# Kernel tuning notes

Hardware: AMD Instinct MI355X
Metric: run time of the kernel (lower is better)

The kernel has to match this reference:

```python
import jax, jax.numpy as jnp
import numpy as np

RADIUS = 0.2  # ball_query_radius
K = 64        # max_group_size


def _xavier(key, out_c, in_c):
    lim = float(np.sqrt(6.0 / (in_c + out_c)))
    return jax.random.uniform(key, (out_c, in_c), jnp.float32, -lim, lim)


def setup_inputs() -> dict:
    key = jax.random.key(0)
    ks = jax.random.split(key, 9)
    B, N, C_in, C_out = 8, 4096, 64, 256
    h = C_out // 2
    return {
        "points": jax.random.uniform(ks[0], (B, 3, N), jnp.float32),
        "point_features": jax.random.normal(ks[1], (B, C_in, N), jnp.float32),
        # point_point_net: Conv2d(3,C_in,1) -> ReLU -> Conv2d(C_in,C_in,1) -> ReLU -> Conv2d(C_in,h,1)
        "pw1": _xavier(ks[2], C_in, 3), "pb1": jnp.zeros(C_in, jnp.float32),
        "pw2": _xavier(ks[3], C_in, C_in), "pb2": jnp.zeros(C_in, jnp.float32),
        "pw3": _xavier(ks[4], h, C_in), "pb3": jnp.zeros(h, jnp.float32),
        # feature_point_net: Conv2d(C_in,C_in,1) -> ReLU -> Conv2d(C_in,C_in,1) -> ReLU -> Conv2d(C_in,h,1)
        "fw1": _xavier(ks[5], C_in, C_in), "fb1": jnp.zeros(C_in, jnp.float32),
        "fw2": _xavier(ks[6], C_in, C_in), "fb2": jnp.zeros(C_in, jnp.float32),
        "fw3": _xavier(ks[7], h, C_in), "fb3": jnp.zeros(h, jnp.float32),
    }


def _fps(pts, M):
    """Farthest point sampling: pts [N,3] -> M int32 indices (first pick = 0)."""
    N = pts.shape[0]

    def step(carry, _):
        mind, last = carry
        d = jnp.sum((pts - pts[last]) ** 2, axis=-1)
        mind = jnp.minimum(mind, d)
        nxt = jnp.argmax(mind).astype(jnp.int32)
        return (mind, nxt), last

    init = (jnp.full((N,), jnp.inf, pts.dtype), jnp.int32(0))
    _, idx = jax.lax.scan(step, init, None, length=M)
    return idx


def _ball_group(cent, pts):
    """cent [M,3], pts [N,3] -> first K in-radius neighbor indices [M,K] (padded with first hit)."""
    N = pts.shape[0]
    d2 = jnp.sum((cent[:, None, :] - pts[None, :, :]) ** 2, axis=-1)  # [M,N]
    score = jnp.where(d2 <= RADIUS * RADIUS, jnp.arange(N, dtype=jnp.int32), N)
    neg_top, _ = jax.lax.top_k(-score, K)     # K smallest scores = first K in-radius point ids
    sel = -neg_top                            # [M,K]
    sel = jnp.where(sel < N, sel, sel[:, :1]) # pad misses with first valid (centroid itself, dist 0)
    return sel


def _mlp3(x, w1, b1, w2, b2, w3, b3):
    """1x1 Conv2d stack applied along the channel axis; x [B,M,K,C]."""
    h = jax.nn.relu(jnp.einsum('bmkc,oc->bmko', x, w1) + b1)
    h = jax.nn.relu(jnp.einsum('bmkc,oc->bmko', h, w2) + b2)
    return jnp.einsum('bmkc,oc->bmko', h, w3) + b3


def reference(points, point_features, pw1, pb1, pw2, pb2, pw3, pb3,
              fw1, fb1, fw2, fb2, fw3, fb3):
    B, _, N = points.shape
    M = N // 4
    pts = points.transpose(0, 2, 1)            # [B,N,3]
    feats = point_features.transpose(0, 2, 1)  # [B,N,C]

    idx = jax.vmap(lambda p: _fps(p, M))(pts)                 # [B,M]
    cent = jnp.take_along_axis(pts, idx[:, :, None], axis=1)  # [B,M,3]
    sel = jax.vmap(_ball_group)(cent, pts)                    # [B,M,K]

    gpts = jax.vmap(lambda p, s: p[s])(pts, sel)              # [B,M,K,3]
    rel = gpts - cent[:, :, None, :]                          # local coords around centroid
    gfeat = jax.vmap(lambda f, s: f[s])(feats, sel)           # [B,M,K,C]

    p_out = jnp.max(_mlp3(rel, pw1, pb1, pw2, pb2, pw3, pb3), axis=2)    # [B,M,h]
    f_out = jnp.max(_mlp3(gfeat, fw1, fb1, fw2, fb2, fw3, fb3), axis=2)  # [B,M,h]

    centroid_features = jnp.concatenate([f_out, p_out], axis=-1).transpose(0, 2, 1)  # [B,C_out,M]
    centroids = cent.reshape(B, 3, M)  # replicates torch .view(B,3,-1) on the flat [B*M,3] buffer
    return centroids, centroid_features
```

## Files before the change

kernel.cpp:

```cpp
#include <hip/hip_runtime.h>
#include <hip/hip_bf16.h>

#define BB   8
#define NN   4096
#define MM   1024
#define KK   64
#define CIN  64
#define HH   128

#define R2F 0.039999999105930328f

#define NPROD (BB + (BB * NN) / 256)
#define H2SU  36
#define SMEMF 21504

static __device__ __forceinline__ float rnd_bf16(float v) {
    return __bfloat162float(__float2bfloat16(v));
}
static __device__ __forceinline__ unsigned int bf16bits(float v) {
    unsigned int u = __float_as_uint(v);
    return (u + 0x7FFFu + ((u >> 16) & 1u)) >> 16;
}
static __device__ __forceinline__ void wavefence() {
    __builtin_amdgcn_wave_barrier();
    __threadfence_block();
    __builtin_amdgcn_wave_barrier();
}

__global__ __launch_bounds__(256) void fused_kernel(
    const float* __restrict__ pts,
    float* __restrict__ centf,
    float* __restrict__ outc,
    const float* __restrict__ feat,
    const float* __restrict__ fw1, const float* __restrict__ fb1,
    const float* __restrict__ fw2, const float* __restrict__ fb2,
    const float* __restrict__ fw3, const float* __restrict__ fb3,
    __hip_bfloat16* __restrict__ fout,
    const float* __restrict__ pw1, const float* __restrict__ pb1,
    const float* __restrict__ pw2, const float* __restrict__ pb2,
    const float* __restrict__ pw3, const float* __restrict__ pb3,
    float* __restrict__ outf,
    unsigned int* __restrict__ flags)
{
    __shared__ float smem[SMEMF];
    __shared__ unsigned long long akey[4];
    const int t = threadIdx.x;

    if (blockIdx.x < BB) {
        const int b = blockIdx.x;
        float* lx = smem;
        float* ly = smem + NN;
        float* lz = smem + 2 * NN;

        const float* px = pts + (size_t)b * 3 * NN;
        float x[16], y[16], z[16], mind[16];
#pragma unroll
        for (int i = 0; i < 16; ++i) {
            int p = t + i * 256;
            x[i] = px[p];
            y[i] = px[NN + p];
            z[i] = px[2 * NN + p];
            lx[p] = x[i]; ly[p] = y[i]; lz[p] = z[i];
            mind[i] = 3.4e38f;
        }
        if (t < 4) akey[t] = 0ULL;
        __syncthreads();

        float bx = lx[0], by = ly[0], bz = lz[0];

        for (int j = 0; j < MM; ++j) {
            if (t == 0) {
                int o = (b * MM + j) * 3;
                centf[o]    = bx; centf[o + 1] = by; centf[o + 2] = bz;
                outc[o]     = rnd_bf16(bx);
                outc[o + 1] = rnd_bf16(by);
                outc[o + 2] = rnd_bf16(bz);
                if ((j & 15) == 15)
                    __hip_atomic_store(&flags[b], (unsigned int)(j + 1),
                                       __ATOMIC_RELEASE, __HIP_MEMORY_SCOPE_AGENT);
                akey[(j + 2) & 3] = 0ULL;
            }
            float bd = -1.0f; int bi = 0;
#pragma unroll
            for (int i = 0; i < 16; ++i) {
                float dx = x[i] - bx, dy = y[i] - by, dz = z[i] - bz;
                float d = __fadd_rn(__fadd_rn(__fmul_rn(dx, dx), __fmul_rn(dy, dy)),
                                    __fmul_rn(dz, dz));
                float md = fminf(mind[i], d);
                mind[i] = md;
                if (md > bd) { bd = md; bi = t + i * 256; }
            }
            unsigned long long key =
                ((unsigned long long)__float_as_uint(bd) << 32) |
                (unsigned long long)(0xFFFFFFFFu - (unsigned)bi);
            atomicMax(&akey[j & 3], key);
            __syncthreads();
            unsigned long long bk = akey[j & 3];
            int best = (int)(0xFFFFFFFFu - (unsigned)(bk & 0xFFFFFFFFULL));
            bx = lx[best]; by = ly[best]; bz = lz[best];
        }
    } else if (blockIdx.x < NPROD) {
        float* w1 = smem;
        float* w2 = smem + CIN * CIN;
        for (int i = t; i < CIN * CIN; i += 256) { w1[i] = fw1[i]; w2[i] = fw2[i]; }
        __syncthreads();

        const int gid = (blockIdx.x - BB) * 256 + t;
        const int b = gid >> 12, n = gid & (NN - 1);
        const float* fp = feat + (size_t)b * CIN * NN + n;

        float f[CIN];
#pragma unroll
        for (int c = 0; c < CIN; ++c) f[c] = fp[(size_t)c * NN];

        float h1[CIN];
        for (int o = 0; o < CIN; ++o) {
            float acc = fb1[o];
#pragma unroll
            for (int c = 0; c < CIN; ++c) acc = fmaf(f[c], w1[o * CIN + c], acc);
            h1[o] = fmaxf(acc, 0.f);
        }
        float h2[CIN];
        for (int o = 0; o < CIN; ++o) {
            float acc = fb2[o];
#pragma unroll
            for (int c = 0; c < CIN; ++c) acc = fmaf(h1[c], w2[o * CIN + c], acc);
            h2[o] = fmaxf(acc, 0.f);
        }
        __hip_bfloat16* op = fout + (size_t)gid * HH;
        for (int o = 0; o < HH; ++o) {
            float acc = fb3[o];
#pragma unroll
            for (int c = 0; c < CIN; ++c) acc = fmaf(h2[c], fw3[o * CIN + c], acc);
            op[o] = __float2bfloat16(acc);
        }
        __threadfence();
        __syncthreads();
        if (t == 0)
            __hip_atomic_fetch_add(&flags[8], 1u,
                                   __ATOMIC_RELEASE, __HIP_MEMORY_SCOPE_AGENT);
    } else {
        const int wv = t >> 6, lane = t & 63;
        unsigned int* h2w = ((unsigned int*)smem) + wv * (KK * H2SU);
        int* selw = ((int*)smem) + 4 * (KK * H2SU) + wv * KK;

        const int idx = blockIdx.x - NPROD;
        const int b = idx & 7;
        const int m = (idx >> 3) * 4 + wv;
        const int g = b * MM + m;

        while (__hip_atomic_load(&flags[b], __ATOMIC_RELAXED,
                                 __HIP_MEMORY_SCOPE_AGENT) <= (unsigned)m)
            __builtin_amdgcn_s_sleep(8);
        (void)__hip_atomic_load(&flags[b], __ATOMIC_ACQUIRE,
                                __HIP_MEMORY_SCOPE_AGENT);

        const float* pts_b = pts + (size_t)b * 3 * NN;
        const float cx = centf[(size_t)g * 3];
        const float cy = centf[(size_t)g * 3 + 1];
        const float cz = centf[(size_t)g * 3 + 2];

        int cnt = 0, first = 0;
        bool have_first = false;
        float fx[4], fy[4], fz[4];
#pragma unroll
        for (int q = 0; q < 4; ++q) {
            int p = q * 64 + lane;
            fx[q] = pts_b[p]; fy[q] = pts_b[NN + p]; fz[q] = pts_b[2 * NN + p];
        }
        for (int base = 0; base < NN; base += 256) {
#pragma unroll
            for (int q = 0; q < 4; ++q) {
                const int cb = base + q * 64;
                float vx = fx[q], vy = fy[q], vz = fz[q];
                const int pre = cb + 256 + lane;
                if (pre < NN) {
                    fx[q] = pts_b[pre]; fy[q] = pts_b[NN + pre]; fz[q] = pts_b[2 * NN + pre];
                }
                float dx = vx - cx, dy = vy - cy, dz = vz - cz;
                float d2 = __fadd_rn(__fadd_rn(__fmul_rn(dx, dx), __fmul_rn(dy, dy)),
                                     __fmul_rn(dz, dz));
                bool in = (d2 <= R2F);
                unsigned long long mask = __ballot(in);
                if (!have_first && mask != 0ULL) {
                    first = cb + (int)__builtin_ctzll(mask);
                    have_first = true;
                }
                int pos = cnt + (int)__popcll(mask & ((1ULL << lane) - 1ULL));
                if (in && pos < KK) selw[pos] = cb + lane;
                cnt += (int)__popcll(mask);
            }
        }
        if (cnt < KK) {
            for (int q = cnt + lane; q < KK; q += 64) selw[q] = first;
        }
        wavefence();

        const int s = selw[lane];
        float* ob = outf + (size_t)b * 256 * MM + m;

        {
            const float x = pts_b[s]          - cx;
            const float y = pts_b[NN + s]     - cy;
            const float z = pts_b[2 * NN + s] - cz;
            float h1[CIN];
#pragma unroll
            for (int o = 0; o < CIN; ++o) {
                float acc = pb1[o];
                acc = fmaf(x, pw1[o * 3 + 0], acc);
                acc = fmaf(y, pw1[o * 3 + 1], acc);
                acc = fmaf(z, pw1[o * 3 + 2], acc);
                h1[o] = fmaxf(acc, 0.f);
            }
            for (int o8 = 0; o8 < CIN / 8; ++o8) {
                float a[8];
#pragma unroll
                for (int q = 0; q < 8; ++q) a[q] = pb2[o8 * 8 + q];
                for (int c = 0; c < CIN; ++c) {
                    float hc = h1[c];
#pragma unroll
                    for (int q = 0; q < 8; ++q)
                        a[q] = fmaf(hc, pw2[(o8 * 8 + q) * CIN + c], a[q]);
                }
                uint4 pk;
                pk.x = bf16bits(fmaxf(a[0], 0.f)) | (bf16bits(fmaxf(a[1], 0.f)) << 16);
                pk.y = bf16bits(fmaxf(a[2], 0.f)) | (bf16bits(fmaxf(a[3], 0.f)) << 16);
                pk.z = bf16bits(fmaxf(a[4], 0.f)) | (bf16bits(fmaxf(a[5], 0.f)) << 16);
                pk.w = bf16bits(fmaxf(a[6], 0.f)) | (bf16bits(fmaxf(a[7], 0.f)) << 16);
                *(uint4*)&h2w[lane * H2SU + o8 * 4] = pk;
            }
        }
        wavefence();

        {
            float w3a[CIN], w3b[CIN];
#pragma unroll
            for (int c = 0; c < CIN; ++c) {
                w3a[c] = pw3[(size_t)lane * CIN + c];
                w3b[c] = pw3[(size_t)(lane + 64) * CIN + c];
            }
            const float b3a = pb3[lane], b3b = pb3[lane + 64];
            float pa0 = -3.4e38f, pb0 = -3.4e38f;
            float pa1 = -3.4e38f, pb1v = -3.4e38f;
            for (int k = 0; k < KK / 2; ++k) {
                float va0 = b3a, vb0 = b3b, va1 = b3a, vb1 = b3b;
#pragma unroll
                for (int u4 = 0; u4 < 8; ++u4) {
                    uint4 p0 = *(const uint4*)&h2w[k * H2SU + u4 * 4];
                    uint4 p1 = *(const uint4*)&h2w[(k + 32) * H2SU + u4 * 4];
                    const unsigned int* w0 = &p0.x;
                    const unsigned int* w1 = &p1.x;
#pragma unroll
                    for (int jj = 0; jj < 4; ++jj) {
                        int c = u4 * 8 + jj * 2;
                        float h0lo = __uint_as_float(w0[jj] << 16);
                        float h0hi = __uint_as_float(w0[jj] & 0xFFFF0000u);
                        float h1lo = __uint_as_float(w1[jj] << 16);
                        float h1hi = __uint_as_float(w1[jj] & 0xFFFF0000u);
                        va0 = fmaf(h0lo, w3a[c],     va0); vb0 = fmaf(h0lo, w3b[c],     vb0);
                        va1 = fmaf(h1lo, w3a[c],     va1); vb1 = fmaf(h1lo, w3b[c],     vb1);
                        va0 = fmaf(h0hi, w3a[c + 1], va0); vb0 = fmaf(h0hi, w3b[c + 1], vb0);
                        va1 = fmaf(h1hi, w3a[c + 1], va1); vb1 = fmaf(h1hi, w3b[c + 1], vb1);
                    }
                }
                pa0 = fmaxf(pa0, va0); pb0  = fmaxf(pb0,  vb0);
                pa1 = fmaxf(pa1, va1); pb1v = fmaxf(pb1v, vb1);
            }
            ob[(size_t)(128 + lane) * MM] = rnd_bf16(fmaxf(pa0, pa1));
            ob[(size_t)(192 + lane) * MM] = rnd_bf16(fmaxf(pb0, pb1v));
        }

        while (__hip_atomic_load(&flags[8], __ATOMIC_RELAXED,
                                 __HIP_MEMORY_SCOPE_AGENT) < (unsigned)(NPROD - BB))
            __builtin_amdgcn_s_sleep(8);
        (void)__hip_atomic_load(&flags[8], __ATOMIC_ACQUIRE,
                                __HIP_MEMORY_SCOPE_AGENT);
        {
            const __hip_bfloat16* fb_ = fout + (size_t)b * NN * HH;
            unsigned int pf[4];
#pragma unroll
            for (int q = 0; q < 4; ++q)
                pf[q] = ((const unsigned int*)(fb_ + (size_t)selw[q] * HH))[lane];
            float alo[4], ahi[4];
#pragma unroll
            for (int q = 0; q < 4; ++q) { alo[q] = -3.4e38f; ahi[q] = -3.4e38f; }
            for (int k = 0; k < KK; k += 4) {
#pragma unroll
                for (int q = 0; q < 4; ++q) {
                    unsigned int wversion = pf[q];
                    int nk = k + 4 + q;
                    if (nk < KK)
                        pf[q] = ((const unsigned int*)(fb_ + (size_t)selw[nk] * HH))[lane];
                    alo[q] = fmaxf(alo[q], __uint_as_float(wversion << 16));
                    ahi[q] = fmaxf(ahi[q], __uint_as_float(wversion & 0xFFFF0000u));
                }
            }
            float lo = fmaxf(fmaxf(alo[0], alo[1]), fmaxf(alo[2], alo[3]));
            float hi = fmaxf(fmaxf(ahi[0], ahi[1]), fmaxf(ahi[2], ahi[3]));
            ob[(size_t)(2 * lane) * MM]     = lo;
            ob[(size_t)(2 * lane + 1) * MM] = hi;
        }
    }
}

extern "C" void kernel_launch(void* const* d_in, const int* in_sizes, int n_in,
                              void* d_out, int out_size, void* d_ws, size_t ws_size,
                              hipStream_t stream) {
    const float* pts  = (const float*)d_in[0];
    const float* feat = (const float*)d_in[1];
    const float* pw1  = (const float*)d_in[2];
    const float* pb1  = (const float*)d_in[3];
    const float* pw2  = (const float*)d_in[4];
    const float* pb2  = (const float*)d_in[5];
    const float* pw3  = (const float*)d_in[6];
    const float* pb3  = (const float*)d_in[7];
    const float* fw1  = (const float*)d_in[8];
    const float* fb1  = (const float*)d_in[9];
    const float* fw2  = (const float*)d_in[10];
    const float* fb2  = (const float*)d_in[11];
    const float* fw3  = (const float*)d_in[12];
    const float* fb3  = (const float*)d_in[13];

    float* out = (float*)d_out;

    float* centf = (float*)d_ws;
    __hip_bfloat16* fout = (__hip_bfloat16*)((char*)d_ws + (size_t)BB * MM * 3 * 4);
    unsigned int* flags = (unsigned int*)((char*)d_ws + (size_t)BB * MM * 3 * 4
                                          + (size_t)BB * NN * HH * 2);

    hipMemsetAsync(flags, 0, 64, stream);

    fused_kernel<<<NPROD + (BB * MM) / 4, 256, 0, stream>>>(
        pts, centf, out, feat, fw1, fb1, fw2, fb2, fw3, fb3, fout,
        pw1, pb1, pw2, pb2, pw3, pb3,
        out + (size_t)BB * MM * 3, flags);
}
```

Baseline: 811.1 us.

## Batch FPS centroid stores via LDS, pad flags apart, and adapt consumer polling

After: 811.0 us. Within noise of the previous version (-0.0%).

```diff
diff --git a/kernel.cpp b/kernel.cpp
--- a/kernel.cpp
+++ b/kernel.cpp
@@ -13,6 +13,8 @@
 #define NPROD (BB + (BB * NN) / 256)
 #define H2SU  36
 #define SMEMF 21504
+#define FLG(b) ((b) * 16)
+#define FDONE  128
 
 static __device__ __forceinline__ float rnd_bf16(float v) {
     return __bfloat162float(__float2bfloat16(v));
@@ -44,6 +46,7 @@
 {
     __shared__ float smem[SMEMF];
     __shared__ unsigned long long akey[4];
+    __shared__ float lsbuf[48];
     const int t = threadIdx.x;
 
     if (blockIdx.x < BB) {
@@ -70,13 +73,11 @@
 
         for (int j = 0; j < MM; ++j) {
             if (t == 0) {
-                int o = (b * MM + j) * 3;
-                centf[o]    = bx; centf[o + 1] = by; centf[o + 2] = bz;
-                outc[o]     = rnd_bf16(bx);
-                outc[o + 1] = rnd_bf16(by);
-                outc[o + 2] = rnd_bf16(bz);
-                if ((j & 15) == 15)
-                    __hip_atomic_store(&flags[b], (unsigned int)(j + 1),
+                lsbuf[(j & 15) * 3 + 0] = bx;
+                lsbuf[(j & 15) * 3 + 1] = by;
+                lsbuf[(j & 15) * 3 + 2] = bz;
+                if ((j & 15) == 1 && j > 16)
+                    __hip_atomic_store(&flags[FLG(b)], (unsigned int)(j - 1),
                                        __ATOMIC_RELEASE, __HIP_MEMORY_SCOPE_AGENT);
                 akey[(j + 2) & 3] = 0ULL;
             }
@@ -95,10 +96,19 @@
                 (unsigned long long)(0xFFFFFFFFu - (unsigned)bi);
             atomicMax(&akey[j & 3], key);
             __syncthreads();
+            if ((j & 15) == 15) {
+                const int base = (b * MM + (j - 15)) * 3;
+                if (t < 48)       centf[base + t]      = lsbuf[t];
+                else if (t < 96)  outc[base + (t - 48)] = rnd_bf16(lsbuf[t - 48]);
+            }
             unsigned long long bk = akey[j & 3];
             int best = (int)(0xFFFFFFFFu - (unsigned)(bk & 0xFFFFFFFFULL));
             bx = lx[best]; by = ly[best]; bz = lz[best];
         }
+        __syncthreads();
+        if (t == 0)
+            __hip_atomic_store(&flags[FLG(b)], (unsigned int)MM,
+                               __ATOMIC_RELEASE, __HIP_MEMORY_SCOPE_AGENT);
     } else if (blockIdx.x < NPROD) {
         float* w1 = smem;
         float* w2 = smem + CIN * CIN;
@@ -137,7 +147,7 @@
         __threadfence();
         __syncthreads();
         if (t == 0)
-            __hip_atomic_fetch_add(&flags[8], 1u,
+            __hip_atomic_fetch_add(&flags[FDONE], 1u,
                                    __ATOMIC_RELEASE, __HIP_MEMORY_SCOPE_AGENT);
     } else {
         const int wv = t >> 6, lane = t & 63;
@@ -149,11 +159,16 @@
         const int m = (idx >> 3) * 4 + wv;
         const int g = b * MM + m;
 
-        while (__hip_atomic_load(&flags[b], __ATOMIC_RELAXED,
-                                 __HIP_MEMORY_SCOPE_AGENT) <= (unsigned)m)
-            __builtin_amdgcn_s_sleep(8);
-        (void)__hip_atomic_load(&flags[b], __ATOMIC_ACQUIRE,
-                                __HIP_MEMORY_SCOPE_AGENT);
+        {
+            unsigned int prog;
+            while ((prog = __hip_atomic_load(&flags[FLG(b)], __ATOMIC_RELAXED,
+                                             __HIP_MEMORY_SCOPE_AGENT)) <= (unsigned)m) {
+                if ((unsigned)m - prog > 128u) __builtin_amdgcn_s_sleep(64);
+                else                           __builtin_amdgcn_s_sleep(8);
+            }
+            (void)__hip_atomic_load(&flags[FLG(b)], __ATOMIC_ACQUIRE,
+                                    __HIP_MEMORY_SCOPE_AGENT);
+        }
 
         const float* pts_b = pts + (size_t)b * 3 * NN;
         const float cx = centf[(size_t)g * 3];
@@ -270,10 +285,10 @@
             ob[(size_t)(192 + lane) * MM] = rnd_bf16(fmaxf(pb0, pb1v));
         }
 
-        while (__hip_atomic_load(&flags[8], __ATOMIC_RELAXED,
+        while (__hip_atomic_load(&flags[FDONE], __ATOMIC_RELAXED,
                                  __HIP_MEMORY_SCOPE_AGENT) < (unsigned)(NPROD - BB))
             __builtin_amdgcn_s_sleep(8);
-        (void)__hip_atomic_load(&flags[8], __ATOMIC_ACQUIRE,
+        (void)__hip_atomic_load(&flags[FDONE], __ATOMIC_ACQUIRE,
                                 __HIP_MEMORY_SCOPE_AGENT);
         {
             const __hip_bfloat16* fb_ = fout + (size_t)b * NN * HH;
@@ -328,7 +343,7 @@
     unsigned int* flags = (unsigned int*)((char*)d_ws + (size_t)BB * MM * 3 * 4
                                           + (size_t)BB * NN * HH * 2);
 
-    hipMemsetAsync(flags, 0, 64, stream);
+    hipMemsetAsync(flags, 0, 1024, stream);
 
     fused_kernel<<<NPROD + (BB * MM) / 4, 256, 0, stream>>>(
         pts, centf, out, feat, fw1, fb1, fw2, fb2, fw3, fb3, fout,
```
